# Kernel tuning notes

Hardware: AMD Instinct MI355X
Metric: run time of the kernel (lower is better)

Reference implementation:

```python
import jax, jax.numpy as jnp
import numpy as np

K = 7          # kernel_size from init
PAD = (K - 1) // 2
EPS = 1e-8


def _local_std(x):
    """Per-pixel std of the zero-padded KxK x C neighborhood, matching
    torch: unfold(pad=3) -> mean over dim=1 (C*K*K) -> sqrt(mean(d^2)+eps).
    Computed with box-filter convolutions instead of materializing the
    49x-blown-up unfold tensor.
    Returns [B, H*W].
    """
    B, C, H, W = x.shape
    n = C * K * K  # fixed divisor (zero padding counts toward the mean)
    ones = jnp.ones((1, C, K, K), x.dtype)  # OIHW: sums over channels + window
    s = jax.lax.conv_general_dilated(x, ones, (1, 1), [(PAD, PAD), (PAD, PAD)])      # [B,1,H,W]
    s2 = jax.lax.conv_general_dilated(x * x, ones, (1, 1), [(PAD, PAD), (PAD, PAD)])  # [B,1,H,W]
    mu = s / n
    var = s2 / n - mu * mu  # E[x^2] - mu^2 == mean((x-mu)^2)
    return jnp.sqrt(var + EPS).reshape(B, H * W)


def _smooth_l1_mean(a, b):
    d = a - b
    ad = jnp.abs(d)
    per = jnp.where(ad < 1.0, 0.5 * d * d, ad - 0.5)
    return jnp.mean(per)


def setup_inputs() -> dict:
    key = jax.random.key(0)
    k1, k2 = jax.random.split(key)
    shape = (16, 3, 512, 512)
    pred_moire = jax.random.normal(k1, shape, dtype=jnp.float32)
    moire = jax.random.normal(k2, shape, dtype=jnp.float32)
    return {"pred_moire": pred_moire, "moire": moire}


def reference(pred_moire, moire):
    std_pred = _local_std(pred_moire)  # [B, H*W]
    std_tgt = _local_std(moire)        # [B, H*W]
    return _smooth_l1_mean(std_pred, std_tgt)  # scalar
```

## Files before the change

kernel.cpp:

```cpp
#include <hip/hip_runtime.h>


#define K     7
#define PAD   3
#define TSX   64
#define TSY   32
#define HR    (TSY + K - 1)
#define LDSW  68
#define NT    256

__device__ __forceinline__ float4 add3(float4 a, float4 b, float4 c) {
    return make_float4(a.x + b.x + c.x, a.y + b.y + c.y,
                       a.z + b.z + c.z, a.w + b.w + c.w);
}
__device__ __forceinline__ float4 sq3(float4 a, float4 b, float4 c) {
    return make_float4(fmaf(a.x, a.x, fmaf(b.x, b.x, c.x * c.x)),
                       fmaf(a.y, a.y, fmaf(b.y, b.y, c.y * c.y)),
                       fmaf(a.z, a.z, fmaf(b.z, b.z, c.z * c.z)),
                       fmaf(a.w, a.w, fmaf(b.w, b.w, c.w * c.w)));
}

__global__ __launch_bounds__(NT, 4) void dist_loss_kernel(
    const float* __restrict__ pred,
    const float* __restrict__ tgt,
    float* __restrict__ out)
{
    constexpr int   C = 3, H = 512, W = 512;
    constexpr float INV_N     = 1.0f / (C * K * K);
    constexpr float INV_TOTAL = 1.0f / (16.0f * 512.0f * 512.0f);

    __shared__ float sh_s[HR][LDSW];
    __shared__ float sh_q[HR][LDSW];

    const int    tid  = threadIdx.x;
    const int    tx0  = blockIdx.x * TSX;
    const int    ty0  = blockIdx.y * TSY;
    const int    b    = blockIdx.z;
    const size_t plane = (size_t)H * W;
    const float4 z4 = make_float4(0.f, 0.f, 0.f, 0.f);

    float4 pA, pB;
    float  acc = 0.0f;

    #pragma unroll
    for (int which = 0; which < 2; ++which) {
        const float* base = (which == 0 ? pred : tgt) + (size_t)b * C * plane;

        for (int task = tid; task < HR * 16; task += NT) {
            const int   row = task >> 4;
            const int   cg  = task & 15;
            const int   gy  = ty0 - PAD + row;
            const float m   = ((unsigned)gy < (unsigned)H) ? 1.0f : 0.0f;
            const int   gyc = min(max(gy, 0), H - 1);
            const int   gx0 = tx0 + (cg << 2);
            const bool  leftOK  = (gx0 > 0);
            const bool  rightOK = (gx0 < 508);

            const float* r0 = base + (size_t)gyc * W + gx0;
            const float* r1 = r0 + plane;
            const float* r2 = r1 + plane;

            float4 A0 = leftOK  ? *(const float4*)(r0 - 4) : z4;
            float4 B0 = *(const float4*)(r0);
            float4 C0 = rightOK ? *(const float4*)(r0 + 4) : z4;
            float4 A1 = leftOK  ? *(const float4*)(r1 - 4) : z4;
            float4 B1 = *(const float4*)(r1);
            float4 C1 = rightOK ? *(const float4*)(r1 + 4) : z4;
            float4 A2 = leftOK  ? *(const float4*)(r2 - 4) : z4;
            float4 B2 = *(const float4*)(r2);
            float4 C2 = rightOK ? *(const float4*)(r2 + 4) : z4;

            float4 tl = add3(A0, A1, A2);
            float4 tm = add3(B0, B1, B2);
            float4 tr = add3(C0, C1, C2);
            float4 ul = sq3(A0, A1, A2);
            float4 um = sq3(B0, B1, B2);
            float4 ur = sq3(C0, C1, C2);

            float h0 = tl.y + tl.z + tl.w + tm.x + tm.y + tm.z + tm.w;
            float h1 = h0 - tl.y + tr.x;
            float h2 = h1 - tl.z + tr.y;
            float h3 = h2 - tl.w + tr.z;
            float g0 = ul.y + ul.z + ul.w + um.x + um.y + um.z + um.w;
            float g1 = g0 - ul.y + ur.x;
            float g2 = g1 - ul.z + ur.y;
            float g3 = g2 - ul.w + ur.z;

            *(float4*)&sh_s[row][cg << 2] =
                make_float4(h0 * m, h1 * m, h2 * m, h3 * m);
            *(float4*)&sh_q[row][cg << 2] =
                make_float4(g0 * m, g1 * m, g2 * m, g3 * m);
        }
        __syncthreads();

        {
            const int rp = tid >> 4;
            const int x  = (tid & 15) << 2;

            float4 S = z4, Q = z4;
            #pragma unroll
            for (int k = 0; k < K; ++k) {
                float4 hv = *(const float4*)&sh_s[2 * rp + k][x];
                float4 gv = *(const float4*)&sh_q[2 * rp + k][x];
                S.x += hv.x; S.y += hv.y; S.z += hv.z; S.w += hv.w;
                Q.x += gv.x; Q.y += gv.y; Q.z += gv.z; Q.w += gv.w;
            }
            float4 hA = *(const float4*)&sh_s[2 * rp][x];
            float4 gA = *(const float4*)&sh_q[2 * rp][x];
            float4 hB = *(const float4*)&sh_s[2 * rp + 7][x];
            float4 gB = *(const float4*)&sh_q[2 * rp + 7][x];
            float4 S2 = make_float4(S.x - hA.x + hB.x, S.y - hA.y + hB.y,
                                    S.z - hA.z + hB.z, S.w - hA.w + hB.w);
            float4 Q2 = make_float4(Q.x - gA.x + gB.x, Q.y - gA.y + gB.y,
                                    Q.z - gA.z + gB.z, Q.w - gA.w + gB.w);

            #define STD4(Sv, Qv, D)                                           \
                {                                                             \
                    float mux = (Sv).x * INV_N, muy = (Sv).y * INV_N,         \
                          muz = (Sv).z * INV_N, muw = (Sv).w * INV_N;         \
                    (D).x = sqrtf(fmaf(-mux, mux, (Qv).x * INV_N) + 1e-8f);   \
                    (D).y = sqrtf(fmaf(-muy, muy, (Qv).y * INV_N) + 1e-8f);   \
                    (D).z = sqrtf(fmaf(-muz, muz, (Qv).z * INV_N) + 1e-8f);   \
                    (D).w = sqrtf(fmaf(-muw, muw, (Qv).w * INV_N) + 1e-8f);   \
                }
            #define SL1(a, bb)                                                \
                {                                                             \
                    float d  = (a) - (bb);                                    \
                    float ad = fabsf(d);                                      \
                    acc += (ad < 1.0f) ? 0.5f * d * d : (ad - 0.5f);          \
                }

            if (which == 0) {
                STD4(S, Q, pA);
                STD4(S2, Q2, pB);
            } else {
                float4 sA, sB;
                STD4(S, Q, sA);
                STD4(S2, Q2, sB);
                SL1(pA.x, sA.x); SL1(pA.y, sA.y);
                SL1(pA.z, sA.z); SL1(pA.w, sA.w);
                SL1(pB.x, sB.x); SL1(pB.y, sB.y);
                SL1(pB.z, sB.z); SL1(pB.w, sB.w);
            }
            #undef STD4
            #undef SL1
        }
        __syncthreads();
    }

    #pragma unroll
    for (int off = 32; off > 0; off >>= 1)
        acc += __shfl_down(acc, off, 64);

    __shared__ float wave_sums[NT / 64];
    if ((tid & 63) == 0) wave_sums[tid >> 6] = acc;
    __syncthreads();
    if (tid == 0) {
        float s = 0.0f;
        #pragma unroll
        for (int w = 0; w < NT / 64; ++w) s += wave_sums[w];
        atomicAdd(out, s * INV_TOTAL);
    }
}

extern "C" void kernel_launch(void* const* d_in, const int* in_sizes, int n_in,
                              void* d_out, int out_size, void* d_ws, size_t ws_size,
                              hipStream_t stream) {
    const float* pred = (const float*)d_in[0];
    const float* tgt  = (const float*)d_in[1];
    float* out = (float*)d_out;

    hipMemsetAsync(out, 0, sizeof(float), stream);

    dim3 grid(512 / TSX, 512 / TSY, 16);
    dist_loss_kernel<<<grid, NT, 0, stream>>>(pred, tgt, out);
}
```

Baseline: 144.9 us.

## Load both inputs in one phase with 8-wide horizontal chunks

Merges the pred and target horizontal-sum phases into a single loop that writes separate LDS buffers, which removes two block barriers and exposes more independent global loads at once. Each task now covers 8 columns using four float4 loads per channel row instead of three, cutting the redundant halo reads from half to a quarter. LDS use doubles with the row padding removed, which may lower occupancy and bring back bank conflicts on the vertical pass.

```diff
diff --git a/kernel.cpp b/kernel.cpp
--- a/kernel.cpp
+++ b/kernel.cpp
@@ -6,8 +6,9 @@
 #define TSX   64
 #define TSY   32
 #define HR    (TSY + K - 1)
-#define LDSW  68
+#define LDSW  64
 #define NT    256
+#define NTASK (2 * HR * 8)
 
 __device__ __forceinline__ float4 add3(float4 a, float4 b, float4 c) {
     return make_float4(a.x + b.x + c.x, a.y + b.y + c.y,
@@ -29,8 +30,8 @@
     constexpr float INV_N     = 1.0f / (C * K * K);
     constexpr float INV_TOTAL = 1.0f / (16.0f * 512.0f * 512.0f);
 
-    __shared__ float sh_s[HR][LDSW];
-    __shared__ float sh_q[HR][LDSW];
+    __shared__ float sh_s[2][HR][LDSW];
+    __shared__ float sh_q[2][HR][LDSW];
 
     const int    tid  = threadIdx.x;
     const int    tx0  = blockIdx.x * TSX;
@@ -39,98 +40,118 @@
     const size_t plane = (size_t)H * W;
     const float4 z4 = make_float4(0.f, 0.f, 0.f, 0.f);
 
-    float4 pA, pB;
-    float  acc = 0.0f;
+    const float* base0 = pred + (size_t)b * C * plane;
+    const float* base1 = tgt  + (size_t)b * C * plane;
 
-    #pragma unroll
-    for (int which = 0; which < 2; ++which) {
-        const float* base = (which == 0 ? pred : tgt) + (size_t)b * C * plane;
+    for (int task = tid; task < NTASK; task += NT) {
+        const int   which = (task >= HR * 8) ? 1 : 0;
+        const int   t     = which ? task - HR * 8 : task;
+        const int   row = t >> 3;
+        const int   cg  = t & 7;
+        const int   gy  = ty0 - PAD + row;
+        const float m   = ((unsigned)gy < (unsigned)H) ? 1.0f : 0.0f;
+        const int   gyc = min(max(gy, 0), H - 1);
+        const int   gx0 = tx0 + (cg << 3);
+        const bool  leftOK  = (gx0 > 0);
+        const bool  rightOK = (gx0 < 504);
 
-        for (int task = tid; task < HR * 16; task += NT) {
-            const int   row = task >> 4;
-            const int   cg  = task & 15;
-            const int   gy  = ty0 - PAD + row;
-            const float m   = ((unsigned)gy < (unsigned)H) ? 1.0f : 0.0f;
-            const int   gyc = min(max(gy, 0), H - 1);
-            const int   gx0 = tx0 + (cg << 2);
-            const bool  leftOK  = (gx0 > 0);
-            const bool  rightOK = (gx0 < 508);
+        const float* base = which ? base1 : base0;
+        const float* r0 = base + (size_t)gyc * W + gx0;
+        const float* r1 = r0 + plane;
+        const float* r2 = r1 + plane;
 
-            const float* r0 = base + (size_t)gyc * W + gx0;
-            const float* r1 = r0 + plane;
-            const float* r2 = r1 + plane;
+        float4 A0 = leftOK  ? *(const float4*)(r0 - 4) : z4;
+        float4 B0 = *(const float4*)(r0);
+        float4 D0 = *(const float4*)(r0 + 4);
+        float4 E0 = rightOK ? *(const float4*)(r0 + 8) : z4;
+        float4 A1 = leftOK  ? *(const float4*)(r1 - 4) : z4;
+        float4 B1 = *(const float4*)(r1);
+        float4 D1 = *(const float4*)(r1 + 4);
+        float4 E1 = rightOK ? *(const float4*)(r1 + 8) : z4;
+        float4 A2 = leftOK  ? *(const float4*)(r2 - 4) : z4;
+        float4 B2 = *(const float4*)(r2);
+        float4 D2 = *(const float4*)(r2 + 4);
+        float4 E2 = rightOK ? *(const float4*)(r2 + 8) : z4;
 
-            float4 A0 = leftOK  ? *(const float4*)(r0 - 4) : z4;
-            float4 B0 = *(const float4*)(r0);
-            float4 C0 = rightOK ? *(const float4*)(r0 + 4) : z4;
-            float4 A1 = leftOK  ? *(const float4*)(r1 - 4) : z4;
-            float4 B1 = *(const float4*)(r1);
-            float4 C1 = rightOK ? *(const float4*)(r1 + 4) : z4;
-            float4 A2 = leftOK  ? *(const float4*)(r2 - 4) : z4;
-            float4 B2 = *(const float4*)(r2);
-            float4 C2 = rightOK ? *(const float4*)(r2 + 4) : z4;
+        float4 tl = add3(A0, A1, A2);
+        float4 ta = add3(B0, B1, B2);
+        float4 tb = add3(D0, D1, D2);
+        float4 tr = add3(E0, E1, E2);
+        float4 ul = sq3(A0, A1, A2);
+        float4 ua = sq3(B0, B1, B2);
+        float4 ub = sq3(D0, D1, D2);
+        float4 ur = sq3(E0, E1, E2);
 
-            float4 tl = add3(A0, A1, A2);
-            float4 tm = add3(B0, B1, B2);
-            float4 tr = add3(C0, C1, C2);
-            float4 ul = sq3(A0, A1, A2);
-            float4 um = sq3(B0, B1, B2);
-            float4 ur = sq3(C0, C1, C2);
+        float h0 = tl.y + tl.z + tl.w + ta.x + ta.y + ta.z + ta.w;
+        float h1 = h0 - tl.y + tb.x;
+        float h2 = h1 - tl.z + tb.y;
+        float h3 = h2 - tl.w + tb.z;
+        float h4 = h3 - ta.x + tb.w;
+        float h5 = h4 - ta.y + tr.x;
+        float h6 = h5 - ta.z + tr.y;
+        float h7 = h6 - ta.w + tr.z;
 
-            float h0 = tl.y + tl.z + tl.w + tm.x + tm.y + tm.z + tm.w;
-            float h1 = h0 - tl.y + tr.x;
-            float h2 = h1 - tl.z + tr.y;
-            float h3 = h2 - tl.w + tr.z;
-            float g0 = ul.y + ul.z + ul.w + um.x + um.y + um.z + um.w;
-            float g1 = g0 - ul.y + ur.x;
-            float g2 = g1 - ul.z + ur.y;
-            float g3 = g2 - ul.w + ur.z;
+        float g0 = ul.y + ul.z + ul.w + ua.x + ua.y + ua.z + ua.w;
+        float g1 = g0 - ul.y + ub.x;
+        float g2 = g1 - ul.z + ub.y;
+        float g3 = g2 - ul.w + ub.z;
+        float g4 = g3 - ua.x + ub.w;
+        float g5 = g4 - ua.y + ur.x;
+        float g6 = g5 - ua.z + ur.y;
+        float g7 = g6 - ua.w + ur.z;
 
-            *(float4*)&sh_s[row][cg << 2] =
-                make_float4(h0 * m, h1 * m, h2 * m, h3 * m);
-            *(float4*)&sh_q[row][cg << 2] =
-                make_float4(g0 * m, g1 * m, g2 * m, g3 * m);
-        }
-        __syncthreads();
+        float* ps = &sh_s[which][row][cg << 3];
+        float* pq = &sh_q[which][row][cg << 3];
+        *(float4*)(ps)     = make_float4(h0 * m, h1 * m, h2 * m, h3 * m);
+        *(float4*)(ps + 4) = make_float4(h4 * m, h5 * m, h6 * m, h7 * m);
+        *(float4*)(pq)     = make_float4(g0 * m, g1 * m, g2 * m, g3 * m);
+        *(float4*)(pq + 4) = make_float4(g4 * m, g5 * m, g6 * m, g7 * m);
+    }
+    __syncthreads();
 
-        {
-            const int rp = tid >> 4;
-            const int x  = (tid & 15) << 2;
+    float acc = 0.0f;
+    {
+        const int rp = tid >> 4;
+        const int x  = (tid & 15) << 2;
 
+        float4 pA, pB;
+
+        #define STD4(Sv, Qv, D)                                           \
+            {                                                             \
+                float mux = (Sv).x * INV_N, muy = (Sv).y * INV_N,         \
+                      muz = (Sv).z * INV_N, muw = (Sv).w * INV_N;         \
+                (D).x = sqrtf(fmaf(-mux, mux, (Qv).x * INV_N) + 1e-8f);   \
+                (D).y = sqrtf(fmaf(-muy, muy, (Qv).y * INV_N) + 1e-8f);   \
+                (D).z = sqrtf(fmaf(-muz, muz, (Qv).z * INV_N) + 1e-8f);   \
+                (D).w = sqrtf(fmaf(-muw, muw, (Qv).w * INV_N) + 1e-8f);   \
+            }
+        #define SL1(a, bb)                                                \
+            {                                                             \
+                float d  = (a) - (bb);                                    \
+                float ad = fabsf(d);                                      \
+                acc += (ad < 1.0f) ? 0.5f * d * d : (ad - 0.5f);          \
+            }
+
+        #pragma unroll
+        for (int w = 0; w < 2; ++w) {
             float4 S = z4, Q = z4;
             #pragma unroll
             for (int k = 0; k < K; ++k) {
-                float4 hv = *(const float4*)&sh_s[2 * rp + k][x];
-                float4 gv = *(const float4*)&sh_q[2 * rp + k][x];
+                float4 hv = *(const float4*)&sh_s[w][2 * rp + k][x];
+                float4 gv = *(const float4*)&sh_q[w][2 * rp + k][x];
                 S.x += hv.x; S.y += hv.y; S.z += hv.z; S.w += hv.w;
                 Q.x += gv.x; Q.y += gv.y; Q.z += gv.z; Q.w += gv.w;
             }
-            float4 hA = *(const float4*)&sh_s[2 * rp][x];
-            float4 gA = *(const float4*)&sh_q[2 * rp][x];
-            float4 hB = *(const float4*)&sh_s[2 * rp + 7][x];
-            float4 gB = *(const float4*)&sh_q[2 * rp + 7][x];
+            float4 hA = *(const float4*)&sh_s[w][2 * rp][x];
+            float4 gA = *(const float4*)&sh_q[w][2 * rp][x];
+            float4 hB = *(const float4*)&sh_s[w][2 * rp + 7][x];
+            float4 gB = *(const float4*)&sh_q[w][2 * rp + 7][x];
             float4 S2 = make_float4(S.x - hA.x + hB.x, S.y - hA.y + hB.y,
                                     S.z - hA.z + hB.z, S.w - hA.w + hB.w);
             float4 Q2 = make_float4(Q.x - gA.x + gB.x, Q.y - gA.y + gB.y,
                                     Q.z - gA.z + gB.z, Q.w - gA.w + gB.w);
 
-            #define STD4(Sv, Qv, D)                                           \
-                {                                                             \
-                    float mux = (Sv).x * INV_N, muy = (Sv).y * INV_N,         \
-                          muz = (Sv).z * INV_N, muw = (Sv).w * INV_N;         \
-                    (D).x = sqrtf(fmaf(-mux, mux, (Qv).x * INV_N) + 1e-8f);   \
-                    (D).y = sqrtf(fmaf(-muy, muy, (Qv).y * INV_N) + 1e-8f);   \
-                    (D).z = sqrtf(fmaf(-muz, muz, (Qv).z * INV_N) + 1e-8f);   \
-                    (D).w = sqrtf(fmaf(-muw, muw, (Qv).w * INV_N) + 1e-8f);   \
-                }
-            #define SL1(a, bb)                                                \
-                {                                                             \
-                    float d  = (a) - (bb);                                    \
-                    float ad = fabsf(d);                                      \
-                    acc += (ad < 1.0f) ? 0.5f * d * d : (ad - 0.5f);          \
-                }
-
-            if (which == 0) {
+            if (w == 0) {
                 STD4(S, Q, pA);
                 STD4(S2, Q2, pB);
             } else {
@@ -142,10 +163,9 @@
                 SL1(pB.x, sB.x); SL1(pB.y, sB.y);
                 SL1(pB.z, sB.z); SL1(pB.w, sB.w);
             }
-            #undef STD4
-            #undef SL1
         }
-        __syncthreads();
+        #undef STD4
+        #undef SL1
     }
 
     #pragma unroll
```

Result: no change. 144.1 us (-0.6%).

## Load both inputs in one pass with double-slotted inline-asm prefetch pipeline

Applied to the files above, without the earlier changes.

Both pred and target tiles are staged into one double-sized shared buffer in a single pass, which removes a barrier round. Each task now covers 8 columns instead of 4. Global loads are issued through inline asm with explicit vmcnt waits, so one slot's loads are in flight while the previous slot is consumed. In exchange, occupancy drops (launch bounds go from 4 to 2 blocks), the LDS padding is removed and may cause bank conflicts, and the hand-scheduled waits are fragile.

```diff
diff --git a/kernel.cpp b/kernel.cpp
--- a/kernel.cpp
+++ b/kernel.cpp
@@ -1,26 +1,27 @@
 #include <hip/hip_runtime.h>
 
+
+typedef float f32x4 __attribute__((ext_vector_type(4)));
 
 #define K     7
 #define PAD   3
 #define TSX   64
 #define TSY   32
 #define HR    (TSY + K - 1)
-#define LDSW  68
+#define LDSW  64
 #define NT    256
-
-__device__ __forceinline__ float4 add3(float4 a, float4 b, float4 c) {
-    return make_float4(a.x + b.x + c.x, a.y + b.y + c.y,
-                       a.z + b.z + c.z, a.w + b.w + c.w);
-}
-__device__ __forceinline__ float4 sq3(float4 a, float4 b, float4 c) {
-    return make_float4(fmaf(a.x, a.x, fmaf(b.x, b.x, c.x * c.x)),
-                       fmaf(a.y, a.y, fmaf(b.y, b.y, c.y * c.y)),
-                       fmaf(a.z, a.z, fmaf(b.z, b.z, c.z * c.z)),
-                       fmaf(a.w, a.w, fmaf(b.w, b.w, c.w * c.w)));
-}
-
-__global__ __launch_bounds__(NT, 4) void dist_loss_kernel(
+#define NTASK (2 * HR * 8)
+
+#define LOADQ(dst, ptr, OFF)                                        \
+    asm volatile("global_load_dwordx4 %0, %1, off offset:" OFF      \
+                 : "=v"(dst) : "v"(ptr))
+
+#define WAITV(N) do {                                               \
+    asm volatile("s_waitcnt vmcnt(" #N ")" ::: "memory");           \
+    __builtin_amdgcn_sched_barrier(0);                              \
+} while (0)
+
+__global__ __launch_bounds__(NT, 2) void dist_loss_kernel(
     const float* __restrict__ pred,
     const float* __restrict__ tgt,
     float* __restrict__ out)
@@ -29,123 +30,165 @@
     constexpr float INV_N     = 1.0f / (C * K * K);
     constexpr float INV_TOTAL = 1.0f / (16.0f * 512.0f * 512.0f);
 
-    __shared__ float sh_s[HR][LDSW];
-    __shared__ float sh_q[HR][LDSW];
+    __shared__ float sh_s[2][HR][LDSW];
+    __shared__ float sh_q[2][HR][LDSW];
 
     const int    tid  = threadIdx.x;
     const int    tx0  = blockIdx.x * TSX;
     const int    ty0  = blockIdx.y * TSY;
     const int    b    = blockIdx.z;
     const size_t plane = (size_t)H * W;
-    const float4 z4 = make_float4(0.f, 0.f, 0.f, 0.f);
-
-    float4 pA, pB;
-    float  acc = 0.0f;
-
-    #pragma unroll
-    for (int which = 0; which < 2; ++which) {
-        const float* base = (which == 0 ? pred : tgt) + (size_t)b * C * plane;
-
-        for (int task = tid; task < HR * 16; task += NT) {
-            const int   row = task >> 4;
-            const int   cg  = task & 15;
-            const int   gy  = ty0 - PAD + row;
-            const float m   = ((unsigned)gy < (unsigned)H) ? 1.0f : 0.0f;
-            const int   gyc = min(max(gy, 0), H - 1);
-            const int   gx0 = tx0 + (cg << 2);
-            const bool  leftOK  = (gx0 > 0);
-            const bool  rightOK = (gx0 < 508);
-
-            const float* r0 = base + (size_t)gyc * W + gx0;
-            const float* r1 = r0 + plane;
-            const float* r2 = r1 + plane;
-
-            float4 A0 = leftOK  ? *(const float4*)(r0 - 4) : z4;
-            float4 B0 = *(const float4*)(r0);
-            float4 C0 = rightOK ? *(const float4*)(r0 + 4) : z4;
-            float4 A1 = leftOK  ? *(const float4*)(r1 - 4) : z4;
-            float4 B1 = *(const float4*)(r1);
-            float4 C1 = rightOK ? *(const float4*)(r1 + 4) : z4;
-            float4 A2 = leftOK  ? *(const float4*)(r2 - 4) : z4;
-            float4 B2 = *(const float4*)(r2);
-            float4 C2 = rightOK ? *(const float4*)(r2 + 4) : z4;
-
-            float4 tl = add3(A0, A1, A2);
-            float4 tm = add3(B0, B1, B2);
-            float4 tr = add3(C0, C1, C2);
-            float4 ul = sq3(A0, A1, A2);
-            float4 um = sq3(B0, B1, B2);
-            float4 ur = sq3(C0, C1, C2);
-
-            float h0 = tl.y + tl.z + tl.w + tm.x + tm.y + tm.z + tm.w;
-            float h1 = h0 - tl.y + tr.x;
-            float h2 = h1 - tl.z + tr.y;
-            float h3 = h2 - tl.w + tr.z;
-            float g0 = ul.y + ul.z + ul.w + um.x + um.y + um.z + um.w;
-            float g1 = g0 - ul.y + ur.x;
-            float g2 = g1 - ul.z + ur.y;
-            float g3 = g2 - ul.w + ur.z;
-
-            *(float4*)&sh_s[row][cg << 2] =
-                make_float4(h0 * m, h1 * m, h2 * m, h3 * m);
-            *(float4*)&sh_q[row][cg << 2] =
-                make_float4(g0 * m, g1 * m, g2 * m, g3 * m);
-        }
-        __syncthreads();
-
-        {
-            const int rp = tid >> 4;
-            const int x  = (tid & 15) << 2;
-
-            float4 S = z4, Q = z4;
+
+    const float* base0 = pred + (size_t)b * C * plane;
+    const float* base1 = tgt  + (size_t)b * C * plane;
+
+    float* shs = &sh_s[0][0][0];
+    float* shq = &sh_q[0][0][0];
+
+    #define DECL_SLOT(S)                                                     \
+        const float *rB0_##S, *rB1_##S, *rB2_##S,                            \
+                    *pA0_##S, *pA1_##S, *pA2_##S,                            \
+                    *pE0_##S, *pE1_##S, *pE2_##S;                            \
+        f32x4 qA0_##S, qB0_##S, qD0_##S, qE0_##S,                            \
+              qA1_##S, qB1_##S, qD1_##S, qE1_##S,                            \
+              qA2_##S, qB2_##S, qD2_##S, qE2_##S;                            \
+        float m_##S, mL_##S, mR_##S; int idx_##S;
+
+    #define SETUP(S, t) do {                                                 \
+        const int which = ((t) >= HR * 8) ? 1 : 0;                           \
+        const int tt    = (t) - which * (HR * 8);                            \
+        const int row   = tt >> 3, cg = tt & 7;                              \
+        const int gy    = ty0 - PAD + row;                                   \
+        m_##S  = ((unsigned)gy < (unsigned)H) ? 1.f : 0.f;                   \
+        const int gyc = min(max(gy, 0), H - 1);                              \
+        const int gx0 = tx0 + (cg << 3);                                     \
+        mL_##S = (gx0 > 0)   ? 1.f : 0.f;                                    \
+        mR_##S = (gx0 < 504) ? 1.f : 0.f;                                    \
+        const float* base = which ? base1 : base0;                           \
+        rB0_##S = base + (size_t)gyc * W + gx0;                              \
+        rB1_##S = rB0_##S + plane;                                           \
+        rB2_##S = rB1_##S + plane;                                           \
+        pA0_##S = rB0_##S + ((gx0 > 0)   ? -4 : 0);                          \
+        pA1_##S = pA0_##S + plane;                                           \
+        pA2_##S = pA1_##S + plane;                                           \
+        pE0_##S = rB0_##S + ((gx0 < 504) ?  4 : 0);     \
+        pE1_##S = pE0_##S + plane;                                           \
+        pE2_##S = pE1_##S + plane;                                           \
+        idx_##S = (which * HR + row) * LDSW + (cg << 3);                     \
+    } while (0)
+
+    #define ISSUE(S) do {                                                    \
+        LOADQ(qA0_##S, pA0_##S, "0");  LOADQ(qB0_##S, rB0_##S, "0");         \
+        LOADQ(qD0_##S, rB0_##S, "16"); LOADQ(qE0_##S, pE0_##S, "16");        \
+        LOADQ(qA1_##S, pA1_##S, "0");  LOADQ(qB1_##S, rB1_##S, "0");         \
+        LOADQ(qD1_##S, rB1_##S, "16"); LOADQ(qE1_##S, pE1_##S, "16");        \
+        LOADQ(qA2_##S, pA2_##S, "0");  LOADQ(qB2_##S, rB2_##S, "0");         \
+        LOADQ(qD2_##S, rB2_##S, "16"); LOADQ(qE2_##S, pE2_##S, "16");        \
+    } while (0)
+
+    #define CONSUME(S) do {                                                  \
+        f32x4 tl = qA0_##S + qA1_##S + qA2_##S;                              \
+        f32x4 ta = qB0_##S + qB1_##S + qB2_##S;                              \
+        f32x4 tb = qD0_##S + qD1_##S + qD2_##S;                              \
+        f32x4 tr = qE0_##S + qE1_##S + qE2_##S;                              \
+        f32x4 ul = qA0_##S*qA0_##S + qA1_##S*qA1_##S + qA2_##S*qA2_##S;      \
+        f32x4 ua = qB0_##S*qB0_##S + qB1_##S*qB1_##S + qB2_##S*qB2_##S;      \
+        f32x4 ub = qD0_##S*qD0_##S + qD1_##S*qD1_##S + qD2_##S*qD2_##S;      \
+        f32x4 ur = qE0_##S*qE0_##S + qE1_##S*qE1_##S + qE2_##S*qE2_##S;      \
+        tl[1] *= mL_##S; tl[2] *= mL_##S; tl[3] *= mL_##S;                   \
+        ul[1] *= mL_##S; ul[2] *= mL_##S; ul[3] *= mL_##S;                   \
+        tr[0] *= mR_##S; tr[1] *= mR_##S; tr[2] *= mR_##S;                   \
+        ur[0] *= mR_##S; ur[1] *= mR_##S; ur[2] *= mR_##S;                   \
+        float h0 = tl[1]+tl[2]+tl[3]+ta[0]+ta[1]+ta[2]+ta[3];                \
+        float h1 = h0 - tl[1] + tb[0];                                       \
+        float h2 = h1 - tl[2] + tb[1];                                       \
+        float h3 = h2 - tl[3] + tb[2];                                       \
+        float h4 = h3 - ta[0] + tb[3];                                       \
+        float h5 = h4 - ta[1] + tr[0];                                       \
+        float h6 = h5 - ta[2] + tr[1];                                       \
+        float h7 = h6 - ta[3] + tr[2];                                       \
+        float g0 = ul[1]+ul[2]+ul[3]+ua[0]+ua[1]+ua[2]+ua[3];                \
+        float g1 = g0 - ul[1] + ub[0];                                       \
+        float g2 = g1 - ul[2] + ub[1];                                       \
+        float g3 = g2 - ul[3] + ub[2];                                       \
+        float g4 = g3 - ua[0] + ub[3];                                       \
+        float g5 = g4 - ua[1] + ur[0];                                       \
+        float g6 = g5 - ua[2] + ur[1];                                       \
+        float g7 = g6 - ua[3] + ur[2];                                       \
+        const float mm = m_##S;                                              \
+        *(f32x4*)&shs[idx_##S]     = (f32x4){h0*mm, h1*mm, h2*mm, h3*mm};    \
+        *(f32x4*)&shs[idx_##S + 4] = (f32x4){h4*mm, h5*mm, h6*mm, h7*mm};    \
+        *(f32x4*)&shq[idx_##S]     = (f32x4){g0*mm, g1*mm, g2*mm, g3*mm};    \
+        *(f32x4*)&shq[idx_##S + 4] = (f32x4){g4*mm, g5*mm, g6*mm, g7*mm};    \
+    } while (0)
+
+    DECL_SLOT(0);
+    DECL_SLOT(1);
+    const int t0 = tid;
+    const int t1 = tid + NT;
+    const int t2 = min(tid + 2 * NT, NTASK - 1);
+
+    SETUP(0, t0); ISSUE(0);
+    SETUP(1, t1); ISSUE(1);
+    WAITV(12);
+    CONSUME(0);
+    SETUP(0, t2); ISSUE(0);
+    WAITV(12);
+    CONSUME(1);
+    WAITV(0);
+    CONSUME(0);
+
+    __syncthreads();
+
+    float acc = 0.0f;
+    {
+        const int rp = tid >> 4;
+        const int x  = (tid & 15) << 2;
+
+        f32x4 pA, pB;
+
+        #define STD4(Sv, Qv, D) do {                                         \
+            _Pragma("unroll")                                                \
+            for (int c_ = 0; c_ < 4; ++c_) {                                 \
+                float mu_ = (Sv)[c_] * INV_N;                                \
+                (D)[c_] = sqrtf(fmaf(-mu_, mu_, (Qv)[c_] * INV_N) + 1e-8f);  \
+            }                                                                \
+        } while (0)
+        #define SL1(a, bb) do {                                              \
+            float d_  = (a) - (bb);                                          \
+            float ad_ = fabsf(d_);                                           \
+            acc += (ad_ < 1.0f) ? 0.5f * d_ * d_ : (ad_ - 0.5f);             \
+        } while (0)
+
+        #pragma unroll
+        for (int w = 0; w < 2; ++w) {
+            f32x4 S = (f32x4){0.f, 0.f, 0.f, 0.f};
+            f32x4 Q = (f32x4){0.f, 0.f, 0.f, 0.f};
             #pragma unroll
             for (int k = 0; k < K; ++k) {
-                float4 hv = *(const float4*)&sh_s[2 * rp + k][x];
-                float4 gv = *(const float4*)&sh_q[2 * rp + k][x];
-                S.x += hv.x; S.y += hv.y; S.z += hv.z; S.w += hv.w;
-                Q.x += gv.x; Q.y += gv.y; Q.z += gv.z; Q.w += gv.w;
+                S += *(const f32x4*)&sh_s[w][2 * rp + k][x];
+                Q += *(const f32x4*)&sh_q[w][2 * rp + k][x];
             }
-            float4 hA = *(const float4*)&sh_s[2 * rp][x];
-            float4 gA = *(const float4*)&sh_q[2 * rp][x];
-            float4 hB = *(const float4*)&sh_s[2 * rp + 7][x];
-            float4 gB = *(const float4*)&sh_q[2 * rp + 7][x];
-            float4 S2 = make_float4(S.x - hA.x + hB.x, S.y - hA.y + hB.y,
-                                    S.z - hA.z + hB.z, S.w - hA.w + hB.w);
-            float4 Q2 = make_float4(Q.x - gA.x + gB.x, Q.y - gA.y + gB.y,
-                                    Q.z - gA.z + gB.z, Q.w - gA.w + gB.w);
-
-            #define STD4(Sv, Qv, D)                                           \
-                {                                                             \
-                    float mux = (Sv).x * INV_N, muy = (Sv).y * INV_N,         \
-                          muz = (Sv).z * INV_N, muw = (Sv).w * INV_N;         \
-                    (D).x = sqrtf(fmaf(-mux, mux, (Qv).x * INV_N) + 1e-8f);   \
-                    (D).y = sqrtf(fmaf(-muy, muy, (Qv).y * INV_N) + 1e-8f);   \
-                    (D).z = sqrtf(fmaf(-muz, muz, (Qv).z * INV_N) + 1e-8f);   \
-                    (D).w = sqrtf(fmaf(-muw, muw, (Qv).w * INV_N) + 1e-8f);   \
-                }
-            #define SL1(a, bb)                                                \
-                {                                                             \
-                    float d  = (a) - (bb);                                    \
-                    float ad = fabsf(d);                                      \
-                    acc += (ad < 1.0f) ? 0.5f * d * d : (ad - 0.5f);          \
-                }
-
-            if (which == 0) {
+            f32x4 S2 = S - *(const f32x4*)&sh_s[w][2 * rp][x]
+                         + *(const f32x4*)&sh_s[w][2 * rp + 7][x];
+            f32x4 Q2 = Q - *(const f32x4*)&sh_q[w][2 * rp][x]
+                         + *(const f32x4*)&sh_q[w][2 * rp + 7][x];
+
+            if (w == 0) {
                 STD4(S, Q, pA);
                 STD4(S2, Q2, pB);
             } else {
-                float4 sA, sB;
+                f32x4 sA, sB;
                 STD4(S, Q, sA);
                 STD4(S2, Q2, sB);
-                SL1(pA.x, sA.x); SL1(pA.y, sA.y);
-                SL1(pA.z, sA.z); SL1(pA.w, sA.w);
-                SL1(pB.x, sB.x); SL1(pB.y, sB.y);
-                SL1(pB.z, sB.z); SL1(pB.w, sB.w);
+                SL1(pA[0], sA[0]); SL1(pA[1], sA[1]);
+                SL1(pA[2], sA[2]); SL1(pA[3], sA[3]);
+                SL1(pB[0], sB[0]); SL1(pB[1], sB[1]);
+                SL1(pB[2], sB[2]); SL1(pB[3], sB[3]);
             }
-            #undef STD4
-            #undef SL1
         }
-        __syncthreads();
+        #undef STD4
+        #undef SL1
     }
 
     #pragma unroll
```

After: 130.2 us. 10.1% less time.

## Warp-specialize into DMA producer and sliding-window consumer waves over full-width row strips

Applied to the files above, without the earlier changes.

Restructures the kernel so each block processes a full-width strip of 16 output rows. Two producer waves stream input rows into LDS with async global_load_lds DMA through a 4-slot ring and reduce the channels. Two consumer waves keep a register ring of horizontal sums and update the vertical 7-tap window incrementally, with both images processed in one pass. This aims to cut the halo re-reads of the 2D tiling and overlap memory traffic with compute. In exchange, occupancy drops to 2 blocks per CU, only half the waves do arithmetic, and every row step needs a block-wide barrier.

```diff
diff --git a/kernel.cpp b/kernel.cpp
--- a/kernel.cpp
+++ b/kernel.cpp
@@ -1,164 +1,190 @@
 #include <hip/hip_runtime.h>
 
 
-#define K     7
-#define PAD   3
-#define TSX   64
-#define TSY   32
-#define HR    (TSY + K - 1)
-#define LDSW  68
-#define NT    256
-
-__device__ __forceinline__ float4 add3(float4 a, float4 b, float4 c) {
-    return make_float4(a.x + b.x + c.x, a.y + b.y + c.y,
-                       a.z + b.z + c.z, a.w + b.w + c.w);
+typedef float f32x4 __attribute__((ext_vector_type(4)));
+
+#define K      7
+#define PAD    3
+#define SH     16
+#define NROW   (SH + K - 1)
+#define DD     3
+#define RS     4
+#define NT     256
+#define IW     512
+#define IH     512
+#define TUW    520
+
+#define WAITV(N) do {                                     \
+    asm volatile("s_waitcnt vmcnt(" #N ")" ::: "memory"); \
+    __builtin_amdgcn_sched_barrier(0);                    \
+} while (0)
+
+__device__ __forceinline__ void dma16(const float* g, float* l) {
+    __builtin_amdgcn_global_load_lds(
+        (const __attribute__((address_space(1))) void*)g,
+        (__attribute__((address_space(3))) void*)l, 16, 0, 0);
 }
-__device__ __forceinline__ float4 sq3(float4 a, float4 b, float4 c) {
-    return make_float4(fmaf(a.x, a.x, fmaf(b.x, b.x, c.x * c.x)),
-                       fmaf(a.y, a.y, fmaf(b.y, b.y, c.y * c.y)),
-                       fmaf(a.z, a.z, fmaf(b.z, b.z, c.z * c.z)),
-                       fmaf(a.w, a.w, fmaf(b.w, b.w, c.w * c.w)));
-}
-
-__global__ __launch_bounds__(NT, 4) void dist_loss_kernel(
+
+__global__ __launch_bounds__(NT, 2) void dist_loss_kernel(
     const float* __restrict__ pred,
     const float* __restrict__ tgt,
     float* __restrict__ out)
 {
-    constexpr int   C = 3, H = 512, W = 512;
-    constexpr float INV_N     = 1.0f / (C * K * K);
+    constexpr float INV_N     = 1.0f / 147.0f;
     constexpr float INV_TOTAL = 1.0f / (16.0f * 512.0f * 512.0f);
 
-    __shared__ float sh_s[HR][LDSW];
-    __shared__ float sh_q[HR][LDSW];
-
-    const int    tid  = threadIdx.x;
-    const int    tx0  = blockIdx.x * TSX;
-    const int    ty0  = blockIdx.y * TSY;
-    const int    b    = blockIdx.z;
-    const size_t plane = (size_t)H * W;
-    const float4 z4 = make_float4(0.f, 0.f, 0.f, 0.f);
-
-    float4 pA, pB;
-    float  acc = 0.0f;
-
+    extern __shared__ float smem[];
+    float* raw_ = smem;
+    float* tu_  = smem + RS * 6 * IW;
+    float* wsum = tu_ + 2 * 2 * 2 * TUW;
+
+    const int  tid  = threadIdx.x;
+    const int  lane = tid & 63;
+    const int  wv   = tid >> 6;
+    const bool prod = (wv < 2);
+    const int  ys   = blockIdx.x * SH;
+    const int  b    = blockIdx.y;
+    const size_t plane = (size_t)IH * IW;
+    const float* base0 = pred + (size_t)b * 3 * plane;
+    const float* base1 = tgt  + (size_t)b * 3 * plane;
+
+    const int hw = wv;
+    const int cp = tid << 2;
+    const int cc = (tid - 128) << 2;
+
+    if (!prod) {
+        int u = tid - 128;
+        if (u < 64) {
+            int row = u >> 3, p = u & 7;
+            tu_[row * TUW + ((p < 4) ? p : (512 + p))] = 0.f;
+        }
+    }
+
+    f32x4 ringh[2][8], ringg[2][8], S[2], Q[2];
     #pragma unroll
-    for (int which = 0; which < 2; ++which) {
-        const float* base = (which == 0 ? pred : tgt) + (size_t)b * C * plane;
-
-        for (int task = tid; task < HR * 16; task += NT) {
-            const int   row = task >> 4;
-            const int   cg  = task & 15;
-            const int   gy  = ty0 - PAD + row;
-            const float m   = ((unsigned)gy < (unsigned)H) ? 1.0f : 0.0f;
-            const int   gyc = min(max(gy, 0), H - 1);
-            const int   gx0 = tx0 + (cg << 2);
-            const bool  leftOK  = (gx0 > 0);
-            const bool  rightOK = (gx0 < 508);
-
-            const float* r0 = base + (size_t)gyc * W + gx0;
-            const float* r1 = r0 + plane;
-            const float* r2 = r1 + plane;
-
-            float4 A0 = leftOK  ? *(const float4*)(r0 - 4) : z4;
-            float4 B0 = *(const float4*)(r0);
-            float4 C0 = rightOK ? *(const float4*)(r0 + 4) : z4;
-            float4 A1 = leftOK  ? *(const float4*)(r1 - 4) : z4;
-            float4 B1 = *(const float4*)(r1);
-            float4 C1 = rightOK ? *(const float4*)(r1 + 4) : z4;
-            float4 A2 = leftOK  ? *(const float4*)(r2 - 4) : z4;
-            float4 B2 = *(const float4*)(r2);
-            float4 C2 = rightOK ? *(const float4*)(r2 + 4) : z4;
-
-            float4 tl = add3(A0, A1, A2);
-            float4 tm = add3(B0, B1, B2);
-            float4 tr = add3(C0, C1, C2);
-            float4 ul = sq3(A0, A1, A2);
-            float4 um = sq3(B0, B1, B2);
-            float4 ur = sq3(C0, C1, C2);
-
-            float h0 = tl.y + tl.z + tl.w + tm.x + tm.y + tm.z + tm.w;
-            float h1 = h0 - tl.y + tr.x;
-            float h2 = h1 - tl.z + tr.y;
-            float h3 = h2 - tl.w + tr.z;
-            float g0 = ul.y + ul.z + ul.w + um.x + um.y + um.z + um.w;
-            float g1 = g0 - ul.y + ur.x;
-            float g2 = g1 - ul.z + ur.y;
-            float g3 = g2 - ul.w + ur.z;
-
-            *(float4*)&sh_s[row][cg << 2] =
-                make_float4(h0 * m, h1 * m, h2 * m, h3 * m);
-            *(float4*)&sh_q[row][cg << 2] =
-                make_float4(g0 * m, g1 * m, g2 * m, g3 * m);
+    for (int wi = 0; wi < 2; ++wi) {
+        S[wi] = (f32x4){0.f, 0.f, 0.f, 0.f};
+        Q[wi] = (f32x4){0.f, 0.f, 0.f, 0.f};
+        #pragma unroll
+        for (int r = 0; r < 8; ++r) {
+            ringh[wi][r] = (f32x4){0.f, 0.f, 0.f, 0.f};
+            ringg[wi][r] = (f32x4){0.f, 0.f, 0.f, 0.f};
         }
-        __syncthreads();
-
-        {
-            const int rp = tid >> 4;
-            const int x  = (tid & 15) << 2;
-
-            float4 S = z4, Q = z4;
-            #pragma unroll
-            for (int k = 0; k < K; ++k) {
-                float4 hv = *(const float4*)&sh_s[2 * rp + k][x];
-                float4 gv = *(const float4*)&sh_q[2 * rp + k][x];
-                S.x += hv.x; S.y += hv.y; S.z += hv.z; S.w += hv.w;
-                Q.x += gv.x; Q.y += gv.y; Q.z += gv.z; Q.w += gv.w;
-            }
-            float4 hA = *(const float4*)&sh_s[2 * rp][x];
-            float4 gA = *(const float4*)&sh_q[2 * rp][x];
-            float4 hB = *(const float4*)&sh_s[2 * rp + 7][x];
-            float4 gB = *(const float4*)&sh_q[2 * rp + 7][x];
-            float4 S2 = make_float4(S.x - hA.x + hB.x, S.y - hA.y + hB.y,
-                                    S.z - hA.z + hB.z, S.w - hA.w + hB.w);
-            float4 Q2 = make_float4(Q.x - gA.x + gB.x, Q.y - gA.y + gB.y,
-                                    Q.z - gA.z + gB.z, Q.w - gA.w + gB.w);
-
-            #define STD4(Sv, Qv, D)                                           \
-                {                                                             \
-                    float mux = (Sv).x * INV_N, muy = (Sv).y * INV_N,         \
-                          muz = (Sv).z * INV_N, muw = (Sv).w * INV_N;         \
-                    (D).x = sqrtf(fmaf(-mux, mux, (Qv).x * INV_N) + 1e-8f);   \
-                    (D).y = sqrtf(fmaf(-muy, muy, (Qv).y * INV_N) + 1e-8f);   \
-                    (D).z = sqrtf(fmaf(-muz, muz, (Qv).z * INV_N) + 1e-8f);   \
-                    (D).w = sqrtf(fmaf(-muw, muw, (Qv).w * INV_N) + 1e-8f);   \
-                }
-            #define SL1(a, bb)                                                \
-                {                                                             \
-                    float d  = (a) - (bb);                                    \
-                    float ad = fabsf(d);                                      \
-                    acc += (ad < 1.0f) ? 0.5f * d * d : (ad - 0.5f);          \
-                }
-
-            if (which == 0) {
-                STD4(S, Q, pA);
-                STD4(S2, Q2, pB);
-            } else {
-                float4 sA, sB;
-                STD4(S, Q, sA);
-                STD4(S2, Q2, sB);
-                SL1(pA.x, sA.x); SL1(pA.y, sA.y);
-                SL1(pA.z, sA.z); SL1(pA.w, sA.w);
-                SL1(pB.x, sB.x); SL1(pB.y, sB.y);
-                SL1(pB.z, sB.z); SL1(pB.w, sB.w);
-            }
-            #undef STD4
-            #undef SL1
+    }
+    float acc = 0.f;
+
+    #define STAGE(rr, slot) do {                                             \
+        const int gy_  = ys - PAD + (rr);                                    \
+        const int gyc_ = min(max(gy_, 0), IH - 1);                           \
+        const float* g0_ = base0 + (size_t)gyc_ * IW + (hw << 8) + (lane << 2); \
+        const float* g1_ = base1 + (size_t)gyc_ * IW + (hw << 8) + (lane << 2); \
+        float* lb_ = raw_ + (slot) * 6 * IW + (hw << 8);                     \
+        dma16(g0_,              lb_);                                        \
+        dma16(g0_ + plane,      lb_ + IW);                                   \
+        dma16(g0_ + 2 * plane,  lb_ + 2 * IW);                               \
+        dma16(g1_,              lb_ + 3 * IW);                               \
+        dma16(g1_ + plane,      lb_ + 4 * IW);                               \
+        dma16(g1_ + 2 * plane,  lb_ + 5 * IW);                               \
+    } while (0)
+
+    #define TUC(i_, SLT, TSL) do {                                           \
+        const int   gy_ = ys - PAD + (i_);                                   \
+        const float m_  = ((unsigned)gy_ < (unsigned)IH) ? 1.f : 0.f;        \
+        const float* rb_ = raw_ + (SLT) * 6 * IW + cp;                       \
+        f32x4 q0 = *(const f32x4*)(rb_);                                     \
+        f32x4 q1 = *(const f32x4*)(rb_ + IW);                                \
+        f32x4 q2 = *(const f32x4*)(rb_ + 2 * IW);                            \
+        f32x4 q3 = *(const f32x4*)(rb_ + 3 * IW);                            \
+        f32x4 q4 = *(const f32x4*)(rb_ + 4 * IW);                            \
+        f32x4 q5 = *(const f32x4*)(rb_ + 5 * IW);                            \
+        f32x4 t0 = (q0 + q1 + q2) * m_;                                      \
+        f32x4 u0 = (q0 * q0 + q1 * q1 + q2 * q2) * m_;                       \
+        f32x4 t1 = (q3 + q4 + q5) * m_;                                      \
+        f32x4 u1 = (q3 * q3 + q4 * q4 + q5 * q5) * m_;                       \
+        float* tb_ = tu_ + (TSL) * (4 * TUW) + cp + 4;                       \
+        *(f32x4*)(tb_)           = t0;                                       \
+        *(f32x4*)(tb_ + TUW)     = u0;                                       \
+        *(f32x4*)(tb_ + 2 * TUW) = t1;                                       \
+        *(f32x4*)(tb_ + 3 * TUW) = u1;                                       \
+    } while (0)
+
+    #define HSLIDE(RB_, HV_) do {                                            \
+        f32x4 a_ = *(const f32x4*)(RB_);                                     \
+        f32x4 b_ = *(const f32x4*)((RB_) + 4);                               \
+        f32x4 c_ = *(const f32x4*)((RB_) + 8);                               \
+        float h0 = a_[1] + a_[2] + a_[3] + b_[0] + b_[1] + b_[2] + b_[3];    \
+        float h1 = h0 - a_[1] + c_[0];                                       \
+        float h2 = h1 - a_[2] + c_[1];                                       \
+        float h3 = h2 - a_[3] + c_[2];                                       \
+        HV_ = (f32x4){h0, h1, h2, h3};                                       \
+    } while (0)
+
+    #define CONS(i_, TSL, JN, JO) do {                                       \
+        const float* tb_ = tu_ + (TSL) * (4 * TUW) + cc;                     \
+        f32x4 hv_;                                                           \
+        HSLIDE(tb_, hv_);                                                    \
+        S[0] += hv_ - ringh[0][JO]; ringh[0][JN] = hv_;                      \
+        HSLIDE(tb_ + TUW, hv_);                                              \
+        Q[0] += hv_ - ringg[0][JO]; ringg[0][JN] = hv_;                      \
+        HSLIDE(tb_ + 2 * TUW, hv_);                                          \
+        S[1] += hv_ - ringh[1][JO]; ringh[1][JN] = hv_;                      \
+        HSLIDE(tb_ + 3 * TUW, hv_);                                          \
+        Q[1] += hv_ - ringg[1][JO]; ringg[1][JN] = hv_;                      \
+        if ((i_) >= 7) {                                                     \
+            _Pragma("unroll")                                                \
+            for (int e_ = 0; e_ < 4; ++e_) {                                 \
+                float mu0 = S[0][e_] * INV_N;                                \
+                float s0_ = sqrtf(fmaf(-mu0, mu0, Q[0][e_] * INV_N) + 1e-8f);\
+                float mu1 = S[1][e_] * INV_N;                                \
+                float s1_ = sqrtf(fmaf(-mu1, mu1, Q[1][e_] * INV_N) + 1e-8f);\
+                float d_  = s0_ - s1_;                                       \
+                float ad_ = fabsf(d_);                                       \
+                acc += (ad_ < 1.f) ? 0.5f * d_ * d_ : (ad_ - 0.5f);          \
+            }                                                                \
+        }                                                                    \
+    } while (0)
+
+    #define ITER(i_, j_, NW_) do {                                           \
+        if (prod) {                                                          \
+            if ((i_) + DD < NROW) STAGE((i_) + DD, ((j_) + DD) & 3);         \
+            WAITV(NW_);                                                      \
+            if ((i_) < NROW) TUC((i_), (j_) & 3, (j_) & 1);                  \
+        } else {                                                             \
+            if ((i_) >= 1) CONS((i_), ((j_) + 1) & 1, ((j_) + 7) & 7, (j_)); \
+        }                                                                    \
+        __syncthreads();                                                     \
+    } while (0)
+
+    if (prod) { STAGE(0, 0); STAGE(1, 1); STAGE(2, 2); }
+
+    #pragma unroll 1
+    for (int g = 0; g < 2; ++g) {
+        #pragma unroll
+        for (int j = 0; j < 8; ++j) {
+            ITER(g * 8 + j, j, 18);
         }
-        __syncthreads();
-    }
+    }
+    ITER(16, 0, 18);
+    ITER(17, 1, 18);
+    ITER(18, 2, 18);
+    ITER(19, 3, 12);
+    ITER(20, 4, 6);
+    ITER(21, 5, 0);
+    ITER(22, 6, 0);
+
+    #undef ITER
+    #undef CONS
+    #undef HSLIDE
+    #undef TUC
+    #undef STAGE
 
     #pragma unroll
     for (int off = 32; off > 0; off >>= 1)
         acc += __shfl_down(acc, off, 64);
-
-    __shared__ float wave_sums[NT / 64];
-    if ((tid & 63) == 0) wave_sums[tid >> 6] = acc;
+    if (lane == 0) wsum[wv] = acc;
     __syncthreads();
     if (tid == 0) {
-        float s = 0.0f;
-        #pragma unroll
-        for (int w = 0; w < NT / 64; ++w) s += wave_sums[w];
+        float s = wsum[0] + wsum[1] + wsum[2] + wsum[3];
         atomicAdd(out, s * INV_TOTAL);
     }
 }
@@ -172,6 +198,8 @@
 
     hipMemsetAsync(out, 0, sizeof(float), stream);
 
-    dim3 grid(512 / TSX, 512 / TSY, 16);
-    dist_loss_kernel<<<grid, NT, 0, stream>>>(pred, tgt, out);
+    const size_t lds_bytes = (RS * 6 * IW + 2 * 2 * 2 * TUW + 4) * sizeof(float);
+
+    dim3 grid(IH / SH, 16);
+    dist_loss_kernel<<<grid, NT, lds_bytes, stream>>>(pred, tgt, out);
 }
```

After: 123.7 us. 1.17x faster.
